# Kernel optimization log

Hardware: AMD Instinct MI355X
Metric: run time of the kernel (lower is better)

## Reference

```python
import jax, jax.numpy as jnp
import numpy as np

B, S = 1, 2048
HID, NH, NKV, HD = 2048, 16, 4, 128
NREP = NH // NKV  # 4
WIN = 1024
ROPE_THETA = 10000.0


def rotate_half(t):
    t1, t2 = jnp.split(t, 2, axis=-1)
    return jnp.concatenate([-t2, t1], axis=-1)


def setup_inputs() -> dict:
    key = jax.random.key(0)
    ks = jax.random.split(key, 5)
    x = jax.random.normal(ks[0], (B, S, HID), dtype=jnp.float32)
    # causal sliding-window additive mask: 0 where attended, -1e9 elsewhere
    i = jnp.arange(S)
    allowed = (i[None, :] <= i[:, None]) & (i[:, None] - i[None, :] < WIN)
    attention_mask = jnp.where(allowed, 0.0, -1e9).astype(jnp.float32)[None, None]  # [1,1,S,S]
    wq = jax.random.normal(ks[1], (NH * HD, HID), dtype=jnp.float32) * 0.02
    wk = jax.random.normal(ks[2], (NKV * HD, HID), dtype=jnp.float32) * 0.02
    wv = jax.random.normal(ks[3], (NKV * HD, HID), dtype=jnp.float32) * 0.02
    wo = jax.random.normal(ks[4], (HID, NH * HD), dtype=jnp.float32) * 0.02
    return {"x": x, "attention_mask": attention_mask, "wq": wq, "wk": wk, "wv": wv, "wo": wo}


def reference(x, attention_mask, wq, wk, wv, wo):
    b, s, _ = x.shape
    q = (x @ wq.T).reshape(b, s, NH, HD)
    k = (x @ wk.T).reshape(b, s, NKV, HD)
    v = (x @ wv.T).reshape(b, s, NKV, HD)
    # rotary embeddings (HF-style rotate_half)
    inv_freq = 1.0 / (ROPE_THETA ** (jnp.arange(0, HD, 2, dtype=jnp.float32) / HD))
    freqs = jnp.arange(s, dtype=jnp.float32)[:, None] * inv_freq[None, :]  # [s, HD/2]
    emb = jnp.concatenate([freqs, freqs], axis=-1)  # [s, HD]
    cos = jnp.cos(emb)[None, :, None, :]
    sin = jnp.sin(emb)[None, :, None, :]
    q = q * cos + rotate_half(q) * sin
    k = k * cos + rotate_half(k) * sin
    # GQA: repeat kv heads
    k = jnp.repeat(k, NREP, axis=2)  # [b, s, NH, HD]
    v = jnp.repeat(v, NREP, axis=2)
    scores = jnp.einsum('bqhd,bkhd->bhqk', q, k) / jnp.sqrt(jnp.float32(HD)) + attention_mask
    probs = jax.nn.softmax(scores.astype(jnp.float32), axis=-1).astype(q.dtype)
    out = jnp.einsum('bhqk,bkhd->bqhd', probs, v).reshape(b, s, NH * HD)
    return out @ wo.T
```

## Files before the change

kernel.cpp:

```cpp
#include <hip/hip_runtime.h>


#define AS1 __attribute__((address_space(1)))
#define AS3 __attribute__((address_space(3)))

typedef short v8s __attribute__((ext_vector_type(8)));
typedef short v4s __attribute__((ext_vector_type(4)));
typedef float v4f __attribute__((ext_vector_type(4)));

__device__ __forceinline__ void gload16(const void* g, void* l) {
  __builtin_amdgcn_global_load_lds((AS1 void*)g, (AS3 void*)l, 16, 0, 0);
}

__device__ __forceinline__ short f2bf(float f) {
  union { float f; unsigned u; } v; v.f = f;
  unsigned r = (v.u + 0x7FFFu + ((v.u >> 16) & 1u)) >> 16;
  return (short)r;
}
__device__ __forceinline__ short f2bf_hu(float f) {
  union { float f; unsigned u; } v; v.f = f;
  return (short)((v.u + 0x8000u) >> 16);
}
__device__ __forceinline__ float bf2f(short h) {
  union { unsigned u; float f; } v; v.u = ((unsigned)(unsigned short)h) << 16;
  return v.f;
}
__device__ __forceinline__ bool sniff_bf16(const unsigned* mask) {
  return mask[1] == 0xCE6ECE6Eu;
}

__device__ __forceinline__ int colmap(int w, int nt, int r) {
  return (w & 1) * 32 + (nt & 1) * 16 + (nt >> 1) * 64 + r;
}

#define ROPE_L2T (13.287712379549449f / 64.0f)
#define Q_SCALE  (1.4426950408889634f * 0.08838834764831845f)
#define SM_SHIFT 8.0f

template <bool BF> struct Raw8;
template <> struct Raw8<true>  { v8s v; };
template <> struct Raw8<false> { float4 a, b; };

template <bool BF> __device__ __forceinline__ Raw8<BF> ldraw(const void* p, size_t e);
template <> __device__ __forceinline__ Raw8<true> ldraw<true>(const void* p, size_t e) {
  Raw8<true> r; r.v = *(const v8s*)((const short*)p + e); return r;
}
template <> __device__ __forceinline__ Raw8<false> ldraw<false>(const void* p, size_t e) {
  Raw8<false> r; const float* f = (const float*)p + e;
  r.a = *(const float4*)f; r.b = *(const float4*)(f + 4); return r;
}
template <bool BF> __device__ __forceinline__ v8s cvt8(const Raw8<BF>& r);
template <> __device__ __forceinline__ v8s cvt8<true>(const Raw8<true>& r) { return r.v; }
template <> __device__ __forceinline__ v8s cvt8<false>(const Raw8<false>& r) {
  v8s o;
  o[0] = f2bf(r.a.x); o[1] = f2bf(r.a.y); o[2] = f2bf(r.a.z); o[3] = f2bf(r.a.w);
  o[4] = f2bf(r.b.x); o[5] = f2bf(r.b.y); o[6] = f2bf(r.b.z); o[7] = f2bf(r.b.w);
  return o;
}

__global__ __launch_bounds__(256) void convert_kernel(
    const void* __restrict__ X, const void* __restrict__ WQ,
    const void* __restrict__ WK, const void* __restrict__ WV,
    const void* __restrict__ WO, const unsigned* __restrict__ mask,
    short* __restrict__ Xbf, short* __restrict__ Wqkvbf, short* __restrict__ WObf)
{
  const bool bf = sniff_bf16(mask);
  size_t e = ((size_t)blockIdx.x * 256 + threadIdx.x) * 8;
  const void* src; short* dst; size_t off, doff;
  if (e < 4194304)       { src = X;  dst = Xbf;  off = e; doff = e; }
  else if (e < 10485760) {
    size_t wv = e - 4194304; dst = Wqkvbf; doff = wv;
    if (wv < 4194304)      { src = WQ; off = wv; }
    else if (wv < 5242880) { src = WK; off = wv - 4194304; }
    else                   { src = WV; off = wv - 5242880; }
  }
  else                   { src = WO; dst = WObf; off = e - 10485760; doff = off; }
  v8s v = bf ? ldraw<true>(src, off).v : cvt8<false>(ldraw<false>(src, off));
  *(v8s*)&dst[doff] = v;
}

__device__ __forceinline__ void gemm_dma_loop(
    const short* __restrict__ A, const short* __restrict__ Bt,
    int m0, int brow0, short* lA, short* lB, v4f acc[2][4])
{
  const int tid = threadIdx.x;
  const int w = tid >> 6, lane = tid & 63;
  const int quad = lane >> 4, r = lane & 15;
  const int wm = (w >> 1) * 32;
  const int rlo = lane >> 2, c8 = (lane & 3) * 8;

  size_t ga[2]; short* la[2];
#pragma unroll
  for (int j = 0; j < 2; ++j) {
    int cA = w * 2 + j;
    int p = cA >> 2, local = cA & 3;
    ga[j] = (size_t)(m0 + local * 16 + rlo) * 2048 + p * 32 + c8;
    la[j] = lA + cA * 512;
  }
  size_t gb[4]; short* lb[4];
#pragma unroll
  for (int j = 0; j < 4; ++j) {
    int cB = w * 4 + j;
    int p = cB >> 3, local = cB & 7;
    gb[j] = (size_t)(brow0 + local * 16 + rlo) * 2048 + p * 32 + c8;
    lb[j] = lB + cB * 512;
  }

  for (int k0 = 0; k0 < 2048; k0 += 64) {
    if (k0) __syncthreads();
#pragma unroll
    for (int j = 0; j < 2; ++j) gload16(A + ga[j] + k0, la[j]);
#pragma unroll
    for (int j = 0; j < 4; ++j) gload16(Bt + gb[j] + k0, lb[j]);
    __syncthreads();
#pragma unroll
    for (int ks = 0; ks < 2; ++ks) {
      v8s a[2], b[4];
#pragma unroll
      for (int mt = 0; mt < 2; ++mt)
        a[mt] = *(const v8s*)&lA[ks * 2048 + (wm + mt * 16 + r) * 32 + quad * 8];
#pragma unroll
      for (int nt = 0; nt < 4; ++nt)
        b[nt] = *(const v8s*)&lB[ks * 4096 + colmap(w, nt, r) * 32 + quad * 8];
#pragma unroll
      for (int mt = 0; mt < 2; ++mt)
#pragma unroll
        for (int nt = 0; nt < 4; ++nt)
          acc[mt][nt] = __builtin_amdgcn_mfma_f32_16x16x32_bf16(a[mt], b[nt], acc[mt][nt], 0, 0, 0);
    }
  }
}

__device__ __forceinline__ void qkv_epilogue(
    v4f acc[2][4], int m0, int n0, short* Qo, short* Ko, short* VTo)
{
  const int tid = threadIdx.x;
  const int w = tid >> 6, lane = tid & 63;
  const int quad = lane >> 4, r = lane & 15;
  const int wm = (w >> 1) * 32;
  const int rowb = m0 + wm + quad * 4;

  if (n0 < 2560) {
    const bool isQ = (n0 < 2048);
    short* dst = isQ ? Qo : Ko;
    const int ld = isQ ? 2048 : 512;
    const int base = isQ ? n0 : (n0 - 2048);
    const float sc = isQ ? Q_SCALE : 1.0f;
#pragma unroll
    for (int nt = 0; nt < 2; ++nt) {
      int d = (w & 1) * 32 + nt * 16 + r;
      float inv = exp2f(-(float)d * ROPE_L2T);
#pragma unroll
      for (int mt = 0; mt < 2; ++mt)
#pragma unroll
        for (int i = 0; i < 4; ++i) {
          int row = rowb + mt * 16 + i;
          float ang = (float)row * inv;
          float cs = cosf(ang), sn = sinf(ang);
          float x1 = acc[mt][nt][i], x2 = acc[mt][nt + 2][i];
          dst[(size_t)row * ld + base + d]      = f2bf((x1 * cs - x2 * sn) * sc);
          dst[(size_t)row * ld + base + d + 64] = f2bf((x2 * cs + x1 * sn) * sc);
        }
    }
  } else {
#pragma unroll
    for (int mt = 0; mt < 2; ++mt)
#pragma unroll
      for (int nt = 0; nt < 4; ++nt) {
        int row = rowb + mt * 16;
        int vcol = n0 - 2560 + colmap(w, nt, r);
        v4s pk;
#pragma unroll
        for (int i = 0; i < 4; ++i) pk[i] = f2bf(acc[mt][nt][i]);
        *(v4s*)&VTo[(size_t)vcol * 2048 + row] = pk;
      }
  }
}

__global__ __launch_bounds__(256, 3) void gemm_qkv_dma(
    const short* __restrict__ Xbf, const short* __restrict__ Wqkvbf,
    short* __restrict__ Qo, short* __restrict__ Ko, short* __restrict__ VTo)
{
  __shared__ __align__(16) short lA[64 * 64];
  __shared__ __align__(16) short lB[128 * 64];
  const int m0 = blockIdx.x * 64;
  const int n0 = blockIdx.y * 128;
  v4f acc[2][4];
#pragma unroll
  for (int i = 0; i < 2; ++i)
#pragma unroll
    for (int j = 0; j < 4; ++j) acc[i][j] = v4f{0.f, 0.f, 0.f, 0.f};
  gemm_dma_loop(Xbf, Wqkvbf, m0, n0, lA, lB, acc);
  qkv_epilogue(acc, m0, n0, Qo, Ko, VTo);
}

__global__ __launch_bounds__(256, 3) void gemm_out_dma(
    const short* __restrict__ A, const short* __restrict__ WObf,
    const unsigned* __restrict__ mask, void* __restrict__ Out)
{
  __shared__ __align__(16) short lA[64 * 64];
  __shared__ __align__(16) short lB[128 * 64];
  const int m0 = blockIdx.x * 64;
  const int n0 = blockIdx.y * 128;
  v4f acc[2][4];
#pragma unroll
  for (int i = 0; i < 2; ++i)
#pragma unroll
    for (int j = 0; j < 4; ++j) acc[i][j] = v4f{0.f, 0.f, 0.f, 0.f};
  gemm_dma_loop(A, WObf, m0, n0, lA, lB, acc);

  const bool bf = sniff_bf16(mask);
  const int tid = threadIdx.x;
  const int w = tid >> 6, lane = tid & 63;
  const int quad = lane >> 4, r = lane & 15;
  const int wm = (w >> 1) * 32;
  const int rowb = m0 + wm + quad * 4;
#pragma unroll
  for (int mt = 0; mt < 2; ++mt)
#pragma unroll
    for (int nt = 0; nt < 4; ++nt) {
      int row = rowb + mt * 16;
      int col = n0 + colmap(w, nt, r);
#pragma unroll
      for (int i = 0; i < 4; ++i) {
        size_t idx = (size_t)(row + i) * 2048 + col;
        if (bf) ((short*)Out)[idx] = f2bf(acc[mt][nt][i]);
        else    ((float*)Out)[idx] = acc[mt][nt][i];
      }
    }
}

template <bool BFA, bool BFB>
__device__ __forceinline__ void gemm64x128_loop(
    const void* __restrict__ A, const void* __restrict__ Bt,
    int m0, int brow0, short* lA, short* lB, v4f acc[2][4])
{
  const int tid = threadIdx.x;
  const int w = tid >> 6, lane = tid & 63;
  const int quad = lane >> 4, r = lane & 15;
  const int wm = (w >> 1) * 32;

  int uoffA[2]; size_t ea[2];
#pragma unroll
  for (int j = 0; j < 2; ++j) {
    int u = tid + 256 * j;
    int row = u >> 3, c = (u & 7) * 8;
    uoffA[j] = (c & 32) * 64 + row * 32 + (c & 31);
    ea[j] = (size_t)(m0 + row) * 2048 + c;
  }
  int uoffB[4]; size_t eb[4];
#pragma unroll
  for (int j = 0; j < 4; ++j) {
    int u = tid + 256 * j;
    int row = u >> 3, c = (u & 7) * 8;
    uoffB[j] = (c & 32) * 128 + row * 32 + (c & 31);
    eb[j] = (size_t)(brow0 + row) * 2048 + c;
  }

  for (int k0 = 0; k0 < 2048; k0 += 64) {
    Raw8<BFA> ta[2]; Raw8<BFB> tb[4];
#pragma unroll
    for (int j = 0; j < 2; ++j) ta[j] = ldraw<BFA>(A, ea[j] + k0);
#pragma unroll
    for (int j = 0; j < 4; ++j) tb[j] = ldraw<BFB>(Bt, eb[j] + k0);
    if (k0) __syncthreads();
#pragma unroll
    for (int j = 0; j < 2; ++j) *(v8s*)&lA[uoffA[j]] = cvt8<BFA>(ta[j]);
#pragma unroll
    for (int j = 0; j < 4; ++j) *(v8s*)&lB[uoffB[j]] = cvt8<BFB>(tb[j]);
    __syncthreads();
#pragma unroll
    for (int ks = 0; ks < 2; ++ks) {
      v8s a[2], b[4];
#pragma unroll
      for (int mt = 0; mt < 2; ++mt)
        a[mt] = *(const v8s*)&lA[ks * 2048 + (wm + mt * 16 + r) * 32 + quad * 8];
#pragma unroll
      for (int nt = 0; nt < 4; ++nt)
        b[nt] = *(const v8s*)&lB[ks * 4096 + colmap(w, nt, r) * 32 + quad * 8];
#pragma unroll
      for (int mt = 0; mt < 2; ++mt)
#pragma unroll
        for (int nt = 0; nt < 4; ++nt)
          acc[mt][nt] = __builtin_amdgcn_mfma_f32_16x16x32_bf16(a[mt], b[nt], acc[mt][nt], 0, 0, 0);
    }
  }
}

__global__ __launch_bounds__(256, 3) void gemm_qkv_fb(
    const void* __restrict__ X, const void* __restrict__ WQ,
    const void* __restrict__ WK, const void* __restrict__ WV,
    const unsigned* __restrict__ mask,
    short* __restrict__ Qo, short* __restrict__ Ko, short* __restrict__ VTo)
{
  __shared__ __align__(16) short lA[64 * 64];
  __shared__ __align__(16) short lB[128 * 64];
  const int m0 = blockIdx.x * 64;
  const int n0 = blockIdx.y * 128;
  const void* Bt; int brow0;
  if (n0 < 2048)      { Bt = WQ; brow0 = n0; }
  else if (n0 < 2560) { Bt = WK; brow0 = n0 - 2048; }
  else                { Bt = WV; brow0 = n0 - 2560; }

  v4f acc[2][4];
#pragma unroll
  for (int i = 0; i < 2; ++i)
#pragma unroll
    for (int j = 0; j < 4; ++j) acc[i][j] = v4f{0.f, 0.f, 0.f, 0.f};

  if (sniff_bf16(mask)) gemm64x128_loop<true, true>(X, Bt, m0, brow0, lA, lB, acc);
  else                  gemm64x128_loop<false, false>(X, Bt, m0, brow0, lA, lB, acc);
  qkv_epilogue(acc, m0, n0, Qo, Ko, VTo);
}

__global__ __launch_bounds__(256, 3) void gemm_out_fb(
    const short* __restrict__ A, const void* __restrict__ WO,
    const unsigned* __restrict__ mask, void* __restrict__ Out)
{
  __shared__ __align__(16) short lA[64 * 64];
  __shared__ __align__(16) short lB[128 * 64];
  const bool bf = sniff_bf16(mask);
  const int m0 = blockIdx.x * 64;
  const int n0 = blockIdx.y * 128;

  v4f acc[2][4];
#pragma unroll
  for (int i = 0; i < 2; ++i)
#pragma unroll
    for (int j = 0; j < 4; ++j) acc[i][j] = v4f{0.f, 0.f, 0.f, 0.f};

  if (bf) gemm64x128_loop<true, true>(A, WO, m0, n0, lA, lB, acc);
  else    gemm64x128_loop<true, false>(A, WO, m0, n0, lA, lB, acc);

  const int tid = threadIdx.x;
  const int w = tid >> 6, lane = tid & 63;
  const int quad = lane >> 4, r = lane & 15;
  const int wm = (w >> 1) * 32;
  const int rowb = m0 + wm + quad * 4;
#pragma unroll
  for (int mt = 0; mt < 2; ++mt)
#pragma unroll
    for (int nt = 0; nt < 4; ++nt) {
      int row = rowb + mt * 16;
      int col = n0 + colmap(w, nt, r);
#pragma unroll
      for (int i = 0; i < 4; ++i) {
        size_t idx = (size_t)(row + i) * 2048 + col;
        if (bf) ((short*)Out)[idx] = f2bf(acc[mt][nt][i]);
        else    ((float*)Out)[idx] = acc[mt][nt][i];
      }
    }
}

__global__ __launch_bounds__(256, 1) void attn_kernel(
    const short* __restrict__ Q, const short* __restrict__ Kb,
    const short* __restrict__ VT, short* __restrict__ Ao)
{
  __shared__ __align__(16) short lK[64 * 128];
  __shared__ __align__(16) short lV[128 * 64];
  __shared__ __align__(16) short lP[4][16 * 72];

  const int bx = blockIdx.x;
  const int qb = bx >> 4, h = bx & 15;
  const int hk = h >> 2;
  const int q0 = qb * 64;
  const int tid = threadIdx.x, w = tid >> 6, lane = tid & 63;
  const int quad = lane >> 4, r = lane & 15;
  const int wq0 = q0 + w * 16;
  short* lPw = lP[w];

  v8s qa[4];
#pragma unroll
  for (int ks = 0; ks < 4; ++ks)
    qa[ks] = *(const v8s*)(Q + (size_t)(wq0 + r) * 2048 + h * 128 + ks * 32 + quad * 8);

  v8s ones;
#pragma unroll
  for (int j = 0; j < 8; ++j) ones[j] = (short)0x3F80;

  v4f Oa[8];
#pragma unroll
  for (int dt = 0; dt < 8; ++dt) Oa[dt] = v4f{0.f, 0.f, 0.f, 0.f};
  v4f La = v4f{0.f, 0.f, 0.f, 0.f};

  const int t0 = (q0 >= 1024) ? ((q0 - 1023) >> 6) : 0;
  const int t1 = qb;

  for (int t = t0; t <= t1; ++t) {
    const int key0 = t << 6;
    v8s tK[4], tV[4];
#pragma unroll
    for (int u = 0; u < 4; ++u) {
      int lin = (w * 4 + u) * 64 + lane;
      int krow = lin >> 4, kcc = lin & 15;
      tK[u] = *(const v8s*)(Kb + (size_t)(key0 + krow) * 512 + hk * 128 + ((kcc ^ krow) & 15) * 8);
      int vrow = lin >> 3, vcc = lin & 7;
      tV[u] = *(const v8s*)(VT + (size_t)(hk * 128 + vrow) * 2048 + key0 + ((vcc ^ vrow) & 7) * 8);
    }
    if (t > t0) __syncthreads();
#pragma unroll
    for (int u = 0; u < 4; ++u) {
      int lin = (w * 4 + u) * 64 + lane;
      *(v8s*)&lK[lin * 8] = tK[u];
      *(v8s*)&lV[lin * 8] = tV[u];
    }
    __syncthreads();

    v4f s4[4];
#pragma unroll
    for (int nt = 0; nt < 4; ++nt) s4[nt] = v4f{0.f, 0.f, 0.f, 0.f};
    __builtin_amdgcn_s_setprio(1);
#pragma unroll
    for (int ks = 0; ks < 4; ++ks)
#pragma unroll
      for (int nt = 0; nt < 4; ++nt) {
        v8s bk = *(const v8s*)&lK[(nt * 16 + r) * 128 + (((ks * 4 + quad) ^ r) & 15) * 8];
        s4[nt] = __builtin_amdgcn_mfma_f32_16x16x32_bf16(qa[ks], bk, s4[nt], 0, 0, 0);
      }
    __builtin_amdgcn_s_setprio(0);

    const bool full = (key0 + 63 <= wq0) && (wq0 + 15 - key0 < 1024);

    if (full) {
#pragma unroll
      for (int nt = 0; nt < 4; ++nt)
#pragma unroll
        for (int i = 0; i < 4; ++i)
          lPw[(quad * 4 + i) * 72 + nt * 16 + r] = f2bf_hu(exp2f(s4[nt][i] - SM_SHIFT));
    } else {
#pragma unroll
      for (int nt = 0; nt < 4; ++nt) {
        int d0 = wq0 + quad * 4 - key0 - nt * 16 - r;
#pragma unroll
        for (int i = 0; i < 4; ++i) {
          bool ok = (unsigned)(d0 + i) < 1024u;
          lPw[(quad * 4 + i) * 72 + nt * 16 + r] =
              ok ? f2bf_hu(exp2f(s4[nt][i] - SM_SHIFT)) : (short)0;
        }
      }
    }

    __builtin_amdgcn_s_setprio(1);
#pragma unroll
    for (int ks2 = 0; ks2 < 2; ++ks2) {
      v8s ap = *(const v8s*)&lPw[r * 72 + ks2 * 32 + quad * 8];
      La = __builtin_amdgcn_mfma_f32_16x16x32_bf16(ap, ones, La, 0, 0, 0);
#pragma unroll
      for (int dt = 0; dt < 8; ++dt) {
        v8s bv = *(const v8s*)&lV[(dt * 16 + r) * 64 + (((ks2 * 4 + quad) ^ r) & 7) * 8];
        Oa[dt] = __builtin_amdgcn_mfma_f32_16x16x32_bf16(ap, bv, Oa[dt], 0, 0, 0);
      }
    }
    __builtin_amdgcn_s_setprio(0);
  }

  float invl[4];
#pragma unroll
  for (int i = 0; i < 4; ++i) invl[i] = (La[i] > 0.f) ? 1.0f / La[i] : 0.f;
#pragma unroll
  for (int dt = 0; dt < 8; ++dt)
#pragma unroll
    for (int i = 0; i < 4; ++i) {
      int q = wq0 + quad * 4 + i;
      Ao[(size_t)q * 2048 + h * 128 + dt * 16 + r] = f2bf(Oa[dt][i] * invl[i]);
    }
}

extern "C" void kernel_launch(void* const* d_in, const int* in_sizes, int n_in,
                              void* d_out, int out_size, void* d_ws, size_t ws_size,
                              hipStream_t stream) {
  const void*     x    = d_in[0];
  const unsigned* mask = (const unsigned*)d_in[1];
  const void*     wq   = d_in[2];
  const void*     wk   = d_in[3];
  const void*     wv   = d_in[4];
  const void*     wo   = d_in[5];

  short* Q  = (short*)d_out;
  short* Kb = (short*)d_ws;
  short* VT = Kb + (size_t)1048576;
  short* Ao = VT + (size_t)1048576;

  const size_t NEED = 41943040ull;
  if (ws_size >= NEED) {
    short* Xbf    = Ao + (size_t)4194304;
    short* Wqkvbf = Xbf + (size_t)4194304;
    short* WObf   = Wqkvbf + (size_t)6291456;
    convert_kernel<<<7168, 256, 0, stream>>>(x, wq, wk, wv, wo, mask, Xbf, Wqkvbf, WObf);
    gemm_qkv_dma<<<dim3(32, 24), 256, 0, stream>>>(Xbf, Wqkvbf, Q, Kb, VT);
    attn_kernel<<<512, 256, 0, stream>>>(Q, Kb, VT, Ao);
    gemm_out_dma<<<dim3(32, 16), 256, 0, stream>>>(Ao, WObf, mask, d_out);
  } else {
    gemm_qkv_fb<<<dim3(32, 24), 256, 0, stream>>>(x, wq, wk, wv, mask, Q, Kb, VT);
    attn_kernel<<<512, 256, 0, stream>>>(Q, Kb, VT, Ao);
    gemm_out_fb<<<dim3(32, 16), 256, 0, stream>>>(Ao, wo, mask, d_out);
  }
}
```

Before: 211.3 us.

## Enlarge DMA GEMM tiles to 128x128 with 4x4 MFMA per wave

The QKV and output-projection GEMMs on the DMA path now use 128x128 block tiles instead of 64x128. Each wave computes a 64x32 sub-tile with sixteen scalar accumulators, which doubles MFMA work per LDS fragment load and halves redundant global reads of the B matrix. The grids shrink to 16x24 and 16x16 blocks and occupancy drops to 2 blocks per SM. On a chip with many CUs (MI355X has 256) this leaves fewer blocks than CUs, so under-filling the device is a risk.

```diff
diff --git a/kernel.cpp b/kernel.cpp
--- a/kernel.cpp
+++ b/kernel.cpp
@@ -79,39 +79,159 @@
   *(v8s*)&dst[doff] = v;
 }
 
-__device__ __forceinline__ void gemm_dma_loop(
-    const short* __restrict__ A, const short* __restrict__ Bt,
+#define MM(I, J) acc##I##J = __builtin_amdgcn_mfma_f32_16x16x32_bf16(a##I, b##J, acc##I##J, 0, 0, 0)
+
+#define GEMM128_BODY(Aptr, Bptr) \
+  const int tid = threadIdx.x; \
+  const int w = tid >> 6, lane = tid & 63; \
+  const int quad = lane >> 4, r = lane & 15; \
+  const int wm = (w >> 1) * 64; \
+  const int rlo = lane >> 2, c8 = (lane & 3) * 8; \
+  size_t ga[4]; short* la[4]; size_t gb[4]; short* lb[4]; \
+  _Pragma("unroll") for (int j = 0; j < 4; ++j) { \
+    int cc = w * 4 + j; int p = cc >> 3, local = cc & 7; \
+    ga[j] = (size_t)(m0 + local * 16 + rlo) * 2048 + p * 32 + c8; \
+    la[j] = lA + cc * 512; \
+    gb[j] = (size_t)(n0 + local * 16 + rlo) * 2048 + p * 32 + c8; \
+    lb[j] = lB + cc * 512; } \
+  v4f acc00 = v4f{0.f, 0.f, 0.f, 0.f}; \
+  v4f acc01 = acc00, acc02 = acc00, acc03 = acc00; \
+  v4f acc10 = acc00, acc11 = acc00, acc12 = acc00, acc13 = acc00; \
+  v4f acc20 = acc00, acc21 = acc00, acc22 = acc00, acc23 = acc00; \
+  v4f acc30 = acc00, acc31 = acc00, acc32 = acc00, acc33 = acc00; \
+  for (int k0 = 0; k0 < 2048; k0 += 64) { \
+    if (k0) __syncthreads(); \
+    _Pragma("unroll") for (int j = 0; j < 4; ++j) gload16(Aptr + ga[j] + k0, la[j]); \
+    _Pragma("unroll") for (int j = 0; j < 4; ++j) gload16(Bptr + gb[j] + k0, lb[j]); \
+    __syncthreads(); \
+    _Pragma("unroll") for (int ks = 0; ks < 2; ++ks) { \
+      const int ab = ks * 4096; \
+      v8s a0 = *(const v8s*)&lA[ab + (wm +  0 + r) * 32 + quad * 8]; \
+      v8s a1 = *(const v8s*)&lA[ab + (wm + 16 + r) * 32 + quad * 8]; \
+      v8s a2 = *(const v8s*)&lA[ab + (wm + 32 + r) * 32 + quad * 8]; \
+      v8s a3 = *(const v8s*)&lA[ab + (wm + 48 + r) * 32 + quad * 8]; \
+      v8s b0 = *(const v8s*)&lB[ab + colmap(w, 0, r) * 32 + quad * 8]; \
+      v8s b1 = *(const v8s*)&lB[ab + colmap(w, 1, r) * 32 + quad * 8]; \
+      v8s b2 = *(const v8s*)&lB[ab + colmap(w, 2, r) * 32 + quad * 8]; \
+      v8s b3 = *(const v8s*)&lB[ab + colmap(w, 3, r) * 32 + quad * 8]; \
+      MM(0,0); MM(0,1); MM(0,2); MM(0,3); \
+      MM(1,0); MM(1,1); MM(1,2); MM(1,3); \
+      MM(2,0); MM(2,1); MM(2,2); MM(2,3); \
+      MM(3,0); MM(3,1); MM(3,2); MM(3,3); \
+    } \
+  }
+
+__global__ __launch_bounds__(256, 2) void gemm_qkv_dma(
+    const short* __restrict__ Xbf, const short* __restrict__ Wqkvbf,
+    short* __restrict__ Qo, short* __restrict__ Ko, short* __restrict__ VTo)
+{
+  __shared__ __align__(16) short lA[128 * 64];
+  __shared__ __align__(16) short lB[128 * 64];
+  const int m0 = blockIdx.x * 128;
+  const int n0 = blockIdx.y * 128;
+  GEMM128_BODY(Xbf, Wqkvbf)
+
+  const int rowb = m0 + wm + quad * 4;
+  if (n0 < 2560) {
+    const bool isQ = (n0 < 2048);
+    short* dst = isQ ? Qo : Ko;
+    const int ld = isQ ? 2048 : 512;
+    const int base = isQ ? n0 : (n0 - 2048);
+    const float sc = isQ ? Q_SCALE : 1.0f;
+#define ROPE_ST(MT, NT, X1, X2) { \
+      int d = (w & 1) * 32 + NT * 16 + r; \
+      float inv = exp2f(-(float)d * ROPE_L2T); \
+      _Pragma("unroll") for (int i = 0; i < 4; ++i) { \
+        int row = rowb + MT * 16 + i; \
+        float ang = (float)row * inv; \
+        float cs = cosf(ang), sn = sinf(ang); \
+        float x1 = X1[i], x2 = X2[i]; \
+        dst[(size_t)row * ld + base + d]      = f2bf((x1 * cs - x2 * sn) * sc); \
+        dst[(size_t)row * ld + base + d + 64] = f2bf((x2 * cs + x1 * sn) * sc); } }
+    ROPE_ST(0, 0, acc00, acc02) ROPE_ST(0, 1, acc01, acc03)
+    ROPE_ST(1, 0, acc10, acc12) ROPE_ST(1, 1, acc11, acc13)
+    ROPE_ST(2, 0, acc20, acc22) ROPE_ST(2, 1, acc21, acc23)
+    ROPE_ST(3, 0, acc30, acc32) ROPE_ST(3, 1, acc31, acc33)
+#undef ROPE_ST
+  } else {
+#define VT_ST(MT, NT, A) { \
+      int row = rowb + MT * 16; \
+      int vcol = n0 - 2560 + colmap(w, NT, r); \
+      v4s pk; \
+      _Pragma("unroll") for (int i = 0; i < 4; ++i) pk[i] = f2bf(A[i]); \
+      *(v4s*)&VTo[(size_t)vcol * 2048 + row] = pk; }
+    VT_ST(0, 0, acc00) VT_ST(0, 1, acc01) VT_ST(0, 2, acc02) VT_ST(0, 3, acc03)
+    VT_ST(1, 0, acc10) VT_ST(1, 1, acc11) VT_ST(1, 2, acc12) VT_ST(1, 3, acc13)
+    VT_ST(2, 0, acc20) VT_ST(2, 1, acc21) VT_ST(2, 2, acc22) VT_ST(2, 3, acc23)
+    VT_ST(3, 0, acc30) VT_ST(3, 1, acc31) VT_ST(3, 2, acc32) VT_ST(3, 3, acc33)
+#undef VT_ST
+  }
+}
+
+__global__ __launch_bounds__(256, 2) void gemm_out_dma(
+    const short* __restrict__ A, const short* __restrict__ WObf,
+    const unsigned* __restrict__ mask, void* __restrict__ Out)
+{
+  __shared__ __align__(16) short lA[128 * 64];
+  __shared__ __align__(16) short lB[128 * 64];
+  const int m0 = blockIdx.x * 128;
+  const int n0 = blockIdx.y * 128;
+  GEMM128_BODY(A, WObf)
+
+  const bool bf = sniff_bf16(mask);
+  const int rowb = m0 + wm + quad * 4;
+#define OUT_ST(MT, NT, ACC) { \
+    int row = rowb + MT * 16; \
+    int col = n0 + colmap(w, NT, r); \
+    _Pragma("unroll") for (int i = 0; i < 4; ++i) { \
+      size_t idx = (size_t)(row + i) * 2048 + col; \
+      if (bf) ((short*)Out)[idx] = f2bf(ACC[i]); \
+      else    ((float*)Out)[idx] = ACC[i]; } }
+  OUT_ST(0, 0, acc00) OUT_ST(0, 1, acc01) OUT_ST(0, 2, acc02) OUT_ST(0, 3, acc03)
+  OUT_ST(1, 0, acc10) OUT_ST(1, 1, acc11) OUT_ST(1, 2, acc12) OUT_ST(1, 3, acc13)
+  OUT_ST(2, 0, acc20) OUT_ST(2, 1, acc21) OUT_ST(2, 2, acc22) OUT_ST(2, 3, acc23)
+  OUT_ST(3, 0, acc30) OUT_ST(3, 1, acc31) OUT_ST(3, 2, acc32) OUT_ST(3, 3, acc33)
+#undef OUT_ST
+}
+
+template <bool BFA, bool BFB>
+__device__ __forceinline__ void gemm64x128_loop(
+    const void* __restrict__ A, const void* __restrict__ Bt,
     int m0, int brow0, short* lA, short* lB, v4f acc[2][4])
 {
   const int tid = threadIdx.x;
   const int w = tid >> 6, lane = tid & 63;
   const int quad = lane >> 4, r = lane & 15;
   const int wm = (w >> 1) * 32;
-  const int rlo = lane >> 2, c8 = (lane & 3) * 8;
-
-  size_t ga[2]; short* la[2];
+
+  int uoffA[2]; size_t ea[2];
 #pragma unroll
   for (int j = 0; j < 2; ++j) {
-    int cA = w * 2 + j;
-    int p = cA >> 2, local = cA & 3;
-    ga[j] = (size_t)(m0 + local * 16 + rlo) * 2048 + p * 32 + c8;
-    la[j] = lA + cA * 512;
-  }
-  size_t gb[4]; short* lb[4];
+    int u = tid + 256 * j;
+    int row = u >> 3, c = (u & 7) * 8;
+    uoffA[j] = (c & 32) * 64 + row * 32 + (c & 31);
+    ea[j] = (size_t)(m0 + row) * 2048 + c;
+  }
+  int uoffB[4]; size_t eb[4];
 #pragma unroll
   for (int j = 0; j < 4; ++j) {
-    int cB = w * 4 + j;
-    int p = cB >> 3, local = cB & 7;
-    gb[j] = (size_t)(brow0 + local * 16 + rlo) * 2048 + p * 32 + c8;
-    lb[j] = lB + cB * 512;
+    int u = tid + 256 * j;
+    int row = u >> 3, c = (u & 7) * 8;
+    uoffB[j] = (c & 32) * 128 + row * 32 + (c & 31);
+    eb[j] = (size_t)(brow0 + row) * 2048 + c;
   }
 
   for (int k0 = 0; k0 < 2048; k0 += 64) {
+    Raw8<BFA> ta[2]; Raw8<BFB> tb[4];
+#pragma unroll
+    for (int j = 0; j < 2; ++j) ta[j] = ldraw<BFA>(A, ea[j] + k0);
+#pragma unroll
+    for (int j = 0; j < 4; ++j) tb[j] = ldraw<BFB>(Bt, eb[j] + k0);
     if (k0) __syncthreads();
 #pragma unroll
-    for (int j = 0; j < 2; ++j) gload16(A + ga[j] + k0, la[j]);
-#pragma unroll
-    for (int j = 0; j < 4; ++j) gload16(Bt + gb[j] + k0, lb[j]);
+    for (int j = 0; j < 2; ++j) *(v8s*)&lA[uoffA[j]] = cvt8<BFA>(ta[j]);
+#pragma unroll
+    for (int j = 0; j < 4; ++j) *(v8s*)&lB[uoffB[j]] = cvt8<BFB>(tb[j]);
     __syncthreads();
 #pragma unroll
     for (int ks = 0; ks < 2; ++ks) {
@@ -131,7 +251,7 @@
   }
 }
 
-__device__ __forceinline__ void qkv_epilogue(
+__device__ __forceinline__ void qkv_epilogue_fb(
     v4f acc[2][4], int m0, int n0, short* Qo, short* Ko, short* VTo)
 {
   const int tid = threadIdx.x;
@@ -177,116 +297,6 @@
   }
 }
 
-__global__ __launch_bounds__(256, 3) void gemm_qkv_dma(
-    const short* __restrict__ Xbf, const short* __restrict__ Wqkvbf,
-    short* __restrict__ Qo, short* __restrict__ Ko, short* __restrict__ VTo)
-{
-  __shared__ __align__(16) short lA[64 * 64];
-  __shared__ __align__(16) short lB[128 * 64];
-  const int m0 = blockIdx.x * 64;
-  const int n0 = blockIdx.y * 128;
-  v4f acc[2][4];
-#pragma unroll
-  for (int i = 0; i < 2; ++i)
-#pragma unroll
-    for (int j = 0; j < 4; ++j) acc[i][j] = v4f{0.f, 0.f, 0.f, 0.f};
-  gemm_dma_loop(Xbf, Wqkvbf, m0, n0, lA, lB, acc);
-  qkv_epilogue(acc, m0, n0, Qo, Ko, VTo);
-}
-
-__global__ __launch_bounds__(256, 3) void gemm_out_dma(
-    const short* __restrict__ A, const short* __restrict__ WObf,
-    const unsigned* __restrict__ mask, void* __restrict__ Out)
-{
-  __shared__ __align__(16) short lA[64 * 64];
-  __shared__ __align__(16) short lB[128 * 64];
-  const int m0 = blockIdx.x * 64;
-  const int n0 = blockIdx.y * 128;
-  v4f acc[2][4];
-#pragma unroll
-  for (int i = 0; i < 2; ++i)
-#pragma unroll
-    for (int j = 0; j < 4; ++j) acc[i][j] = v4f{0.f, 0.f, 0.f, 0.f};
-  gemm_dma_loop(A, WObf, m0, n0, lA, lB, acc);
-
-  const bool bf = sniff_bf16(mask);
-  const int tid = threadIdx.x;
-  const int w = tid >> 6, lane = tid & 63;
-  const int quad = lane >> 4, r = lane & 15;
-  const int wm = (w >> 1) * 32;
-  const int rowb = m0 + wm + quad * 4;
-#pragma unroll
-  for (int mt = 0; mt < 2; ++mt)
-#pragma unroll
-    for (int nt = 0; nt < 4; ++nt) {
-      int row = rowb + mt * 16;
-      int col = n0 + colmap(w, nt, r);
-#pragma unroll
-      for (int i = 0; i < 4; ++i) {
-        size_t idx = (size_t)(row + i) * 2048 + col;
-        if (bf) ((short*)Out)[idx] = f2bf(acc[mt][nt][i]);
-        else    ((float*)Out)[idx] = acc[mt][nt][i];
-      }
-    }
-}
-
-template <bool BFA, bool BFB>
-__device__ __forceinline__ void gemm64x128_loop(
-    const void* __restrict__ A, const void* __restrict__ Bt,
-    int m0, int brow0, short* lA, short* lB, v4f acc[2][4])
-{
-  const int tid = threadIdx.x;
-  const int w = tid >> 6, lane = tid & 63;
-  const int quad = lane >> 4, r = lane & 15;
-  const int wm = (w >> 1) * 32;
-
-  int uoffA[2]; size_t ea[2];
-#pragma unroll
-  for (int j = 0; j < 2; ++j) {
-    int u = tid + 256 * j;
-    int row = u >> 3, c = (u & 7) * 8;
-    uoffA[j] = (c & 32) * 64 + row * 32 + (c & 31);
-    ea[j] = (size_t)(m0 + row) * 2048 + c;
-  }
-  int uoffB[4]; size_t eb[4];
-#pragma unroll
-  for (int j = 0; j < 4; ++j) {
-    int u = tid + 256 * j;
-    int row = u >> 3, c = (u & 7) * 8;
-    uoffB[j] = (c & 32) * 128 + row * 32 + (c & 31);
-    eb[j] = (size_t)(brow0 + row) * 2048 + c;
-  }
-
-  for (int k0 = 0; k0 < 2048; k0 += 64) {
-    Raw8<BFA> ta[2]; Raw8<BFB> tb[4];
-#pragma unroll
-    for (int j = 0; j < 2; ++j) ta[j] = ldraw<BFA>(A, ea[j] + k0);
-#pragma unroll
-    for (int j = 0; j < 4; ++j) tb[j] = ldraw<BFB>(Bt, eb[j] + k0);
-    if (k0) __syncthreads();
-#pragma unroll
-    for (int j = 0; j < 2; ++j) *(v8s*)&lA[uoffA[j]] = cvt8<BFA>(ta[j]);
-#pragma unroll
-    for (int j = 0; j < 4; ++j) *(v8s*)&lB[uoffB[j]] = cvt8<BFB>(tb[j]);
-    __syncthreads();
-#pragma unroll
-    for (int ks = 0; ks < 2; ++ks) {
-      v8s a[2], b[4];
-#pragma unroll
-      for (int mt = 0; mt < 2; ++mt)
-        a[mt] = *(const v8s*)&lA[ks * 2048 + (wm + mt * 16 + r) * 32 + quad * 8];
-#pragma unroll
-      for (int nt = 0; nt < 4; ++nt)
-        b[nt] = *(const v8s*)&lB[ks * 4096 + colmap(w, nt, r) * 32 + quad * 8];
-#pragma unroll
-      for (int mt = 0; mt < 2; ++mt)
-#pragma unroll
-        for (int nt = 0; nt < 4; ++nt)
-          acc[mt][nt] = __builtin_amdgcn_mfma_f32_16x16x32_bf16(a[mt], b[nt], acc[mt][nt], 0, 0, 0);
-    }
-  }
-}
-
 __global__ __launch_bounds__(256, 3) void gemm_qkv_fb(
     const void* __restrict__ X, const void* __restrict__ WQ,
     const void* __restrict__ WK, const void* __restrict__ WV,
@@ -310,7 +320,7 @@
 
   if (sniff_bf16(mask)) gemm64x128_loop<true, true>(X, Bt, m0, brow0, lA, lB, acc);
   else                  gemm64x128_loop<false, false>(X, Bt, m0, brow0, lA, lB, acc);
-  qkv_epilogue(acc, m0, n0, Qo, Ko, VTo);
+  qkv_epilogue_fb(acc, m0, n0, Qo, Ko, VTo);
 }
 
 __global__ __launch_bounds__(256, 3) void gemm_out_fb(
@@ -487,9 +497,9 @@
     short* Wqkvbf = Xbf + (size_t)4194304;
     short* WObf   = Wqkvbf + (size_t)6291456;
     convert_kernel<<<7168, 256, 0, stream>>>(x, wq, wk, wv, wo, mask, Xbf, Wqkvbf, WObf);
-    gemm_qkv_dma<<<dim3(32, 24), 256, 0, stream>>>(Xbf, Wqkvbf, Q, Kb, VT);
+    gemm_qkv_dma<<<dim3(16, 24), 256, 0, stream>>>(Xbf, Wqkvbf, Q, Kb, VT);
     attn_kernel<<<512, 256, 0, stream>>>(Q, Kb, VT, Ao);
-    gemm_out_dma<<<dim3(32, 16), 256, 0, stream>>>(Ao, WObf, mask, d_out);
+    gemm_out_dma<<<dim3(16, 16), 256, 0, stream>>>(Ao, WObf, mask, d_out);
   } else {
     gemm_qkv_fb<<<dim3(32, 24), 256, 0, stream>>>(x, wq, wk, wv, mask, Q, Kb, VT);
     attn_kernel<<<512, 256, 0, stream>>>(Q, Kb, VT, Ao);
```

Result: slower. 235.3 us (+11.3%).
